# Kernel tuning notes

Hardware: AMD Instinct MI355X
Metric: run time of the kernel (lower is better)

## Reference

```python
import jax, jax.numpy as jnp
import numpy as np

INPUT_SIZE, HIDDEN_SIZE, MEMORY_SIZE, SEQ_LEN, THETA = 512, 1024, 256, 4096, 4096.0
BATCH = 8


def _expm(M):
    # scaling-and-squaring Taylor expm (float64), replaces scipy cont2discrete's expm
    nrm = np.linalg.norm(M, 1)
    s = max(0, int(np.ceil(np.log2(max(nrm, 1.0)))) + 4)
    A = M / (2.0 ** s)
    E = np.eye(M.shape[0])
    T = np.eye(M.shape[0])
    for k in range(1, 24):
        T = T @ A / k
        E = E + T
    for _ in range(s):
        E = E @ E
    return E


def _lmu_H():
    # continuous-time Legendre state-space matrices
    Q = np.arange(MEMORY_SIZE, dtype=np.float64).reshape(-1, 1)
    R = (2.0 * Q + 1.0) / THETA
    i, j = np.meshgrid(Q.ravel(), Q.ravel(), indexing="ij")
    A = R * np.where(i < j, -1.0, (-1.0) ** (i - j + 1))
    B = R * (-1.0) ** Q
    # zero-order-hold discretization with dt=1: expm([[A,B],[0,0]])
    aug = np.zeros((MEMORY_SIZE + 1, MEMORY_SIZE + 1))
    aug[:MEMORY_SIZE, :MEMORY_SIZE] = A
    aug[:MEMORY_SIZE, MEMORY_SIZE:] = B
    Md = _expm(aug)
    Ad = Md[:MEMORY_SIZE, :MEMORY_SIZE].astype(np.float32)
    Bd = Md[:MEMORY_SIZE, MEMORY_SIZE:].astype(np.float32)
    # impulse response: H[:, t] = Ad^t @ Bd  (matches torch impulse() in float32)
    H = np.empty((MEMORY_SIZE, SEQ_LEN), dtype=np.float32)
    h = Bd[:, 0]
    for t in range(SEQ_LEN):
        H[:, t] = h
        h = Ad @ h
    return H


def setup_inputs():
    key = jax.random.key(0)
    k1, k2, k3, k4, k5 = jax.random.split(key, 5)
    x = jax.random.normal(k1, (BATCH, SEQ_LEN, INPUT_SIZE), jnp.float32)
    W_u_w = jax.random.normal(k2, (1, INPUT_SIZE), jnp.float32) / np.float32(np.sqrt(INPUT_SIZE))
    W_u_b = jax.random.normal(k3, (1,), jnp.float32) * 0.01
    W_h_w = jax.random.normal(k4, (HIDDEN_SIZE, MEMORY_SIZE + INPUT_SIZE), jnp.float32) / np.float32(np.sqrt(MEMORY_SIZE + INPUT_SIZE))
    W_h_b = jax.random.normal(k5, (HIDDEN_SIZE,), jnp.float32) * 0.01
    H = jnp.asarray(_lmu_H())
    return {"x": x, "W_u_w": W_u_w, "W_u_b": W_u_b, "W_h_w": W_h_w, "W_h_b": W_h_b, "H": H}


def reference(x, W_u_w, W_u_b, W_h_w, W_h_b, H):
    B, S, D = x.shape
    # u_t = relu(W_u x_t)  -> [B, S, 1]
    u = jax.nn.relu(jnp.einsum("bsd,od->bso", x, W_u_w) + W_u_b)
    # FFT long convolution of u with impulse response H (linear conv via 2S padding)
    fft_u = jnp.fft.rfft(u.transpose(0, 2, 1), n=2 * S, axis=-1)  # [B, 1, S+1]
    fft_H = jnp.fft.rfft(H, n=2 * S, axis=-1)                     # [M, S+1]
    m = jnp.fft.irfft(fft_u * fft_H[None], n=2 * S, axis=-1)[:, :, :S]  # [B, M, S]
    m = m.transpose(0, 2, 1)                                      # [B, S, M]
    # h_t = relu(W_h [m_t; x_t])
    h = jax.nn.relu(jnp.einsum("bsk,hk->bsh", jnp.concatenate([m, x], axis=-1), W_h_w) + W_h_b)
    return h, h[:, -1, :]
```

## Files before the change

### kernel.cpp

```cpp
#include <hip/hip_runtime.h>

typedef _Float16 half8 __attribute__((ext_vector_type(8)));
typedef float f32x4 __attribute__((ext_vector_type(4)));

#define SEQ   4096
#define DIN   512
#define HID   1024
#define KMEM  256
#define NB    8
#define KC    768
#define VP    4352
#define OUT_H_ELEMS 33554432ull

__device__ __forceinline__ void load_lds16(const void* g, void* l) {
  __builtin_amdgcn_global_load_lds(
      (const __attribute__((address_space(1))) unsigned int*)g,
      (__attribute__((address_space(3))) unsigned int*)l, 16, 0, 0);
}

__global__ __launch_bounds__(256) void u_kernel(
    const float* __restrict__ x, const float* __restrict__ Wu,
    const float* __restrict__ Wub,
    const float* __restrict__ Hf, const float* __restrict__ Wf,
    _Float16* __restrict__ xh, _Float16* __restrict__ v2,
    _Float16* __restrict__ Hh, _Float16* __restrict__ Wh)
{
  int tid_g = blockIdx.x * 256 + threadIdx.x;
  if (tid_g < KMEM * SEQ) Hh[tid_g] = (_Float16)Hf[tid_g];
  if (tid_g < HID * KC)   Wh[tid_g] = (_Float16)Wf[tid_g];
  if (tid_g < NB * 8 * 256) {
    int b2 = tid_g >> 11, rem = tid_g & 2047, p = rem >> 8, z = rem & 255;
    int t = (z < p) ? z : 4096 + z;
    v2[((size_t)b2 * 8 + p) * VP + t] = (_Float16)0.f;
  }

  int w = threadIdx.x >> 6, lane = threadIdx.x & 63;
  int row = blockIdx.x * 4 + w;
  const float4* xr = (const float4*)(x + (size_t)row * DIN);
  const float4* wr = (const float4*)Wu;
  float4 a0 = xr[lane * 2], a1 = xr[lane * 2 + 1];
  float4 w0 = wr[lane * 2], w1 = wr[lane * 2 + 1];
  float dot = a0.x * w0.x + a0.y * w0.y + a0.z * w0.z + a0.w * w0.w
            + a1.x * w1.x + a1.y * w1.y + a1.z * w1.z + a1.w * w1.w;
  half8 hv;
  hv[0] = (_Float16)a0.x; hv[1] = (_Float16)a0.y;
  hv[2] = (_Float16)a0.z; hv[3] = (_Float16)a0.w;
  hv[4] = (_Float16)a1.x; hv[5] = (_Float16)a1.y;
  hv[6] = (_Float16)a1.z; hv[7] = (_Float16)a1.w;
  *((half8*)(xh + (size_t)row * DIN + lane * 8)) = hv;
  #pragma unroll
  for (int off = 32; off > 0; off >>= 1) dot += __shfl_xor(dot, off);
  float u = dot + Wub[0];
  u = u > 0.f ? u : 0.f;
  if (lane < 8) {
    int s = row & (SEQ - 1), b = row >> 12;
    v2[(size_t)b * 8 * VP + (size_t)lane * VP + (4095 - s + lane)] = (_Float16)u;
  }
}

__global__ __launch_bounds__(256, 3) void conv_kernel(
    const _Float16* __restrict__ Hh, const _Float16* __restrict__ v2,
    _Float16* __restrict__ mh)
{
  __shared__ _Float16 Bs[2][128 * 64];
  __shared__ _Float16 Aw[2][8 * 208];
  int g = blockIdx.x;
  int cb = g & 15;
  int b = cb >> 1, kt = cb & 1;
  int jj = g >> 4;
  int its = (jj < 16) ? jj : (47 - jj);
  int s0 = its * 128, k0 = kt * 128;
  int tid = threadIdx.x;
  int w = tid >> 6, lane = tid & 63;
  int wr = w >> 1, wc = w & 1;
  int lm = lane & 15, q = lane >> 4;
  const _Float16* v2b = v2 + (size_t)b * 8 * VP;
  int gb = 3968 - s0;

  int aoffs[4];
  #pragma unroll
  for (int mi = 0; mi < 4; mi++) {
    int X = wr * 64 + mi * 16 + lm;
    int p = (X + 1) & 7;
    aoffs[mi] = p * 208 + (127 - X + p) + q * 8;
  }
  int boffs[4];
  #pragma unroll
  for (int ni = 0; ni < 4; ni++) {
    int col = wc * 64 + ni * 16 + lm;
    boffs[ni] = col * 64 + ((q ^ (lm & 7)) << 3);
  }

  int ap = tid / 26, aidx = tid - ap * 26;

  f32x4 acc[4][4] = {};
  int iters = 2 * (its + 1);

  {
    if (tid < 208)
      load_lds16(v2b + (size_t)ap * VP + gb + aidx * 8, Aw[0] + tid * 8);
    #pragma unroll
    for (int p2 = 0; p2 < 4; p2++) {
      int c = p2 * 256 + tid;
      int col = c >> 3, sl = c & 7;
      load_lds16(Hh + (size_t)(k0 + col) * SEQ + ((sl ^ (col & 7)) << 3),
                 Bs[0] + (size_t)c * 8);
    }
  }

  for (int it = 0; it < iters; ++it) {
    int buf = it & 1;
    __syncthreads();
    if (it + 1 < iters) {
      int r0 = (it + 1) * 64;
      if (tid < 208)
        load_lds16(v2b + (size_t)ap * VP + gb + r0 + aidx * 8, Aw[buf ^ 1] + tid * 8);
      #pragma unroll
      for (int p2 = 0; p2 < 4; p2++) {
        int c = p2 * 256 + tid;
        int col = c >> 3, sl = c & 7;
        load_lds16(Hh + (size_t)(k0 + col) * SEQ + r0 + ((sl ^ (col & 7)) << 3),
                   Bs[buf ^ 1] + (size_t)c * 8);
      }
    }
    #pragma unroll
    for (int kq = 0; kq < 2; kq++) {
      half8 af[4], bf[4];
      #pragma unroll
      for (int mi = 0; mi < 4; mi++)
        af[mi] = *((const half8*)(Aw[buf] + aoffs[mi] + kq * 32));
      #pragma unroll
      for (int ni = 0; ni < 4; ni++)
        bf[ni] = *((const half8*)(Bs[buf] + (boffs[ni] ^ (kq << 5))));
      #pragma unroll
      for (int mi = 0; mi < 4; mi++)
        #pragma unroll
        for (int ni = 0; ni < 4; ni++)
          acc[mi][ni] = __builtin_amdgcn_mfma_f32_16x16x32_f16(af[mi], bf[ni], acc[mi][ni], 0, 0, 0);
    }
  }
  size_t rowbase = (size_t)b * SEQ;
  #pragma unroll
  for (int mi = 0; mi < 4; mi++) {
    #pragma unroll
    for (int ni = 0; ni < 4; ni++) {
      int kout = k0 + wc * 64 + ni * 16 + lm;
      #pragma unroll
      for (int r = 0; r < 4; r++) {
        int sout = s0 + wr * 64 + mi * 16 + q * 4 + r;
        mh[(rowbase + sout) * KMEM + kout] = (_Float16)acc[mi][ni][r];
      }
    }
  }
}

__global__ __launch_bounds__(256) void h_kernel(
    const _Float16* __restrict__ mh, const _Float16* __restrict__ xh,
    const _Float16* __restrict__ Wh, const float* __restrict__ Whb,
    float* __restrict__ out)
{
  __shared__ _Float16 As[2][128 * 32];
  __shared__ _Float16 Bs[2][128 * 32];
  int id = blockIdx.y * 8 + blockIdx.x;
  int xcd = id & 7;
  int j = id >> 3;
  int mt = (j >> 3) * 8 + xcd;
  int nt = j & 7;
  int tid = threadIdx.x, w = tid >> 6, lane = tid & 63;
  int wr = w >> 1, wc = w & 1, lm = lane & 15, q = lane >> 4;

  f32x4 acc[4][4] = {};
  {
    #pragma unroll
    for (int p2 = 0; p2 < 2; p2++) {
      int c = p2 * 256 + tid;
      int row = c >> 2, ch = c & 3;
      size_t rg = (size_t)mt * 128 + row;
      load_lds16(mh + rg * KMEM + ch * 8, As[0] + (size_t)c * 8);
      load_lds16(Wh + (size_t)(nt * 128 + row) * KC + ch * 8, Bs[0] + (size_t)c * 8);
    }
  }
  for (int it = 0; it < 24; ++it) {
    int buf = it & 1;
    __syncthreads();
    if (it + 1 < 24) {
      int kk = (it + 1) * 32;
      #pragma unroll
      for (int p2 = 0; p2 < 2; p2++) {
        int c = p2 * 256 + tid;
        int row = c >> 2, ch = c & 3;
        size_t rg = (size_t)mt * 128 + row;
        const _Float16* srcA = (kk < KMEM)
            ? (mh + rg * KMEM + kk + ch * 8)
            : (xh + rg * DIN + (kk - KMEM) + ch * 8);
        load_lds16(srcA, As[buf ^ 1] + (size_t)c * 8);
        load_lds16(Wh + (size_t)(nt * 128 + row) * KC + kk + ch * 8,
                   Bs[buf ^ 1] + (size_t)c * 8);
      }
    }
    half8 af[4], bf[4];
    #pragma unroll
    for (int mi = 0; mi < 4; mi++)
      af[mi] = *((const half8*)(As[buf] + (wr * 64 + mi * 16 + lm) * 32 + q * 8));
    #pragma unroll
    for (int ni = 0; ni < 4; ni++)
      bf[ni] = *((const half8*)(Bs[buf] + (wc * 64 + ni * 16 + lm) * 32 + q * 8));
    #pragma unroll
    for (int mi = 0; mi < 4; mi++)
      #pragma unroll
      for (int ni = 0; ni < 4; ni++)
        acc[mi][ni] = __builtin_amdgcn_mfma_f32_16x16x32_f16(af[mi], bf[ni], acc[mi][ni], 0, 0, 0);
  }
  #pragma unroll
  for (int ni = 0; ni < 4; ni++) {
    int colg = nt * 128 + wc * 64 + ni * 16 + lm;
    float bias = Whb[colg];
    #pragma unroll
    for (int mi = 0; mi < 4; mi++) {
      #pragma unroll
      for (int r = 0; r < 4; r++) {
        int rowg = mt * 128 + wr * 64 + mi * 16 + q * 4 + r;
        float v = acc[mi][ni][r] + bias;
        v = v > 0.f ? v : 0.f;
        __builtin_nontemporal_store(v, &out[(size_t)rowg * HID + colg]);
        if ((rowg & (SEQ - 1)) == SEQ - 1)
          __builtin_nontemporal_store(
              v, &out[OUT_H_ELEMS + (size_t)(rowg >> 12) * HID + colg]);
      }
    }
  }
}

extern "C" void kernel_launch(void* const* d_in, const int* in_sizes, int n_in,
                              void* d_out, int out_size, void* d_ws, size_t ws_size,
                              hipStream_t stream) {
  const float* x   = (const float*)d_in[0];
  const float* Wu  = (const float*)d_in[1];
  const float* Wub = (const float*)d_in[2];
  const float* Whw = (const float*)d_in[3];
  const float* Whb = (const float*)d_in[4];
  const float* Hf  = (const float*)d_in[5];
  float* out = (float*)d_out;

  char* ws = (char*)d_ws;
  _Float16* Hh = (_Float16*)(ws);
  _Float16* Wh = (_Float16*)(ws + 2097152);
  _Float16* v2 = (_Float16*)(ws + 3670016);
  _Float16* xh = (_Float16*)(ws + 4227072);
  _Float16* mh = (_Float16*)(ws + 37781504);

  u_kernel<<<dim3(8192), dim3(256), 0, stream>>>(x, Wu, Wub, Hf, Whw, xh, v2, Hh, Wh);
  conv_kernel<<<dim3(512), dim3(256), 0, stream>>>(Hh, v2, mh);
  h_kernel<<<dim3(8, 256), dim3(256), 0, stream>>>(mh, xh, Wh, Whb, out);
}
```

Measured before the change: 308.3 us.

## Widen h_kernel tile to 128x256 with 8 waves, swizzled LDS, setprio

The output GEMM now uses 512-thread blocks computing 128x256 tiles instead of 256-thread 128x128 tiles. This halves the number of blocks and the number of A-tile reloads. LDS layout gains an XOR swizzle on the 16-byte chunks to reduce bank conflicts on fragment reads. The block-to-tile mapping is changed for XCD locality, and s_setprio is raised around the MFMA block. LDS per block grows, and occupancy is traded for more reuse.

```diff
diff --git a/kernel.cpp b/kernel.cpp
--- a/kernel.cpp
+++ b/kernel.cpp
@@ -154,66 +154,81 @@
   }
 }
 
-__global__ __launch_bounds__(256) void h_kernel(
+__global__ __launch_bounds__(512, 4) void h_kernel(
     const _Float16* __restrict__ mh, const _Float16* __restrict__ xh,
     const _Float16* __restrict__ Wh, const float* __restrict__ Whb,
     float* __restrict__ out)
 {
   __shared__ _Float16 As[2][128 * 32];
-  __shared__ _Float16 Bs[2][128 * 32];
-  int id = blockIdx.y * 8 + blockIdx.x;
-  int xcd = id & 7;
-  int j = id >> 3;
-  int mt = (j >> 3) * 8 + xcd;
-  int nt = j & 7;
+  __shared__ _Float16 Bs[2][256 * 32];
+  int id = blockIdx.x;
+  int wgid = (id & 7) * 128 + (id >> 3);
+  int mt = wgid >> 2;
+  int nt = wgid & 3;
   int tid = threadIdx.x, w = tid >> 6, lane = tid & 63;
-  int wr = w >> 1, wc = w & 1, lm = lane & 15, q = lane >> 4;
+  int wr = w >> 2, wc = w & 3;
+  int lm = lane & 15, q = lane >> 4;
+
+  int offM, offX;
+  {
+    int rowA = tid >> 2, chA = tid & 3;
+    int swA = chA ^ ((rowA >> 2) & 3);
+    offM = (mt * 128 + rowA) * KMEM + swA * 8;
+    offX = (mt * 128 + rowA) * DIN  + swA * 8;
+  }
+  int offB[2];
+  #pragma unroll
+  for (int r = 0; r < 2; ++r) {
+    int c = r * 512 + tid;
+    int rowB = c >> 2, chB = c & 3;
+    int swB = chB ^ ((rowB >> 2) & 3);
+    offB[r] = (nt * 256 + rowB) * KC + swB * 8;
+  }
+
+  int qs = (q ^ ((lm >> 2) & 3)) << 3;
+  int aoff[4], boff[4];
+  #pragma unroll
+  for (int mi = 0; mi < 4; ++mi) aoff[mi] = (wr * 64 + mi * 16 + lm) * 32 + qs;
+  #pragma unroll
+  for (int ni = 0; ni < 4; ++ni) boff[ni] = (wc * 64 + ni * 16 + lm) * 32 + qs;
 
   f32x4 acc[4][4] = {};
   {
-    #pragma unroll
-    for (int p2 = 0; p2 < 2; p2++) {
-      int c = p2 * 256 + tid;
-      int row = c >> 2, ch = c & 3;
-      size_t rg = (size_t)mt * 128 + row;
-      load_lds16(mh + rg * KMEM + ch * 8, As[0] + (size_t)c * 8);
-      load_lds16(Wh + (size_t)(nt * 128 + row) * KC + ch * 8, Bs[0] + (size_t)c * 8);
-    }
-  }
+    load_lds16(mh + offM, As[0] + tid * 8);
+    #pragma unroll
+    for (int r = 0; r < 2; ++r)
+      load_lds16(Wh + offB[r], Bs[0] + (size_t)(r * 512 + tid) * 8);
+  }
+
   for (int it = 0; it < 24; ++it) {
     int buf = it & 1;
     __syncthreads();
     if (it + 1 < 24) {
       int kk = (it + 1) * 32;
-      #pragma unroll
-      for (int p2 = 0; p2 < 2; p2++) {
-        int c = p2 * 256 + tid;
-        int row = c >> 2, ch = c & 3;
-        size_t rg = (size_t)mt * 128 + row;
-        const _Float16* srcA = (kk < KMEM)
-            ? (mh + rg * KMEM + kk + ch * 8)
-            : (xh + rg * DIN + (kk - KMEM) + ch * 8);
-        load_lds16(srcA, As[buf ^ 1] + (size_t)c * 8);
-        load_lds16(Wh + (size_t)(nt * 128 + row) * KC + kk + ch * 8,
-                   Bs[buf ^ 1] + (size_t)c * 8);
-      }
+      const _Float16* srcA = (kk < KMEM) ? (mh + offM + kk)
+                                         : (xh + offX + (kk - KMEM));
+      load_lds16(srcA, As[buf ^ 1] + tid * 8);
+      #pragma unroll
+      for (int r = 0; r < 2; ++r)
+        load_lds16(Wh + offB[r] + kk, Bs[buf ^ 1] + (size_t)(r * 512 + tid) * 8);
     }
     half8 af[4], bf[4];
     #pragma unroll
-    for (int mi = 0; mi < 4; mi++)
-      af[mi] = *((const half8*)(As[buf] + (wr * 64 + mi * 16 + lm) * 32 + q * 8));
-    #pragma unroll
-    for (int ni = 0; ni < 4; ni++)
-      bf[ni] = *((const half8*)(Bs[buf] + (wc * 64 + ni * 16 + lm) * 32 + q * 8));
-    #pragma unroll
-    for (int mi = 0; mi < 4; mi++)
-      #pragma unroll
-      for (int ni = 0; ni < 4; ni++)
+    for (int mi = 0; mi < 4; ++mi) af[mi] = *((const half8*)(As[buf] + aoff[mi]));
+    #pragma unroll
+    for (int ni = 0; ni < 4; ++ni) bf[ni] = *((const half8*)(Bs[buf] + boff[ni]));
+    __builtin_amdgcn_s_setprio(1);
+    #pragma unroll
+    for (int mi = 0; mi < 4; ++mi)
+      #pragma unroll
+      for (int ni = 0; ni < 4; ++ni)
         acc[mi][ni] = __builtin_amdgcn_mfma_f32_16x16x32_f16(af[mi], bf[ni], acc[mi][ni], 0, 0, 0);
-  }
+    __builtin_amdgcn_s_setprio(0);
+  }
+
   #pragma unroll
   for (int ni = 0; ni < 4; ni++) {
-    int colg = nt * 128 + wc * 64 + ni * 16 + lm;
+    int colg = nt * 256 + wc * 64 + ni * 16 + lm;
     float bias = Whb[colg];
     #pragma unroll
     for (int mi = 0; mi < 4; mi++) {
@@ -251,5 +266,5 @@
 
   u_kernel<<<dim3(8192), dim3(256), 0, stream>>>(x, Wu, Wub, Hf, Whw, xh, v2, Hh, Wh);
   conv_kernel<<<dim3(512), dim3(256), 0, stream>>>(Hh, v2, mh);
-  h_kernel<<<dim3(8, 256), dim3(256), 0, stream>>>(mh, xh, Wh, Whb, out);
-}
+  h_kernel<<<dim3(1024), dim3(512), 0, stream>>>(mh, xh, Wh, Whb, out);
+}
```

Measured after the change: 305.8 us. No clear change (-0.8%).
